# Performance work log

Hardware: AMD Instinct MI355X
Metric: run time of the kernel (lower is better)

The kernel has to match this reference:

```python
import jax, jax.numpy as jnp
import numpy as np

RX = (2, 9)
RY = (4, 9)
G, O = 64, 2          # column chunk size and overlap (hardcoded in original forward)
GK = RX[1]            # Gaussian (uniform box) kernel size, must be odd
M = N = 512


def _patches(x, kh, kw, pc, pr):
    # torch: F.pad(x,(pr,pr,pc,pc)).unfold(-2,kh,1).unfold(-2,kw,1).flatten(-2)
    xp = jnp.pad(x, ((0, 0), (0, 0), (pc, pc), (pr, pr)))
    p = jax.lax.conv_general_dilated_patches(xp, (kh, kw), (1, 1), 'VALID')  # (b, kh*kw, m, n) since c==1
    return jnp.moveaxis(p, 1, -1)[:, None]  # (b,1,m,n,kh*kw)


def _spatial_kernel(kh, kw):
    d = (jnp.arange(kh, dtype=jnp.float32) - kh // 2)[:, None] ** 2 \
        + (jnp.arange(kw, dtype=jnp.float32) - kw // 2)[None, :] ** 2
    return jnp.exp(-d.reshape(-1) / ((kh * kw) / 4.0) ** 2)


def _gen_weight(ych, kh, kw, pc, pr, sigma):
    p = _patches(ych, kh, kw, pc, pr)
    w = jnp.exp(-((p - ych[..., None]) ** 2) / (sigma / 2.0) ** 2)  # range (bilateral) term
    w = w * _spatial_kernel(kh, kw)                                  # spatial Gaussian term
    w = w * _patches(jnp.ones_like(ych), kh, kw, pc, pr)             # zero out padded taps
    return w / w.sum(-1, keepdims=True)


def _boxfilter(x, weight, kh, kw, pc, pr):
    return (_patches(x, kh, kw, pc, pr) * weight).sum(-1)


def _forward(X, y, r):
    sigma = r[0] * (y.max() - y.min())
    kh0, kw0, pc0, pr0 = 2 * RX[0] + 1, 2 * RY[0] + 1, RX[0], RY[0]  # detail kernel
    kh1, kw1, pc1, pr1 = 2 * RX[1] + 1, 2 * RY[1] + 1, RX[1], RY[1]  # base kernel
    gk = jnp.ones((1, 1, GK, GK), X.dtype) / float(GK * GK)
    pad = GK // 2
    conv = lambda z: jax.lax.conv_general_dilated(z, gk, (1, 1), [(pad, pad), (pad, pad)])

    # Angle = [0]: rotate(.,0,expand=True) and CenterCrop(m,n) are identities.
    XX, yy = X, y
    XXbase, yybase = conv(XX), conv(yy)
    XXdetail, yydetail = XX - XXbase, yy - yybase

    n = X.shape[-1]
    idx = np.arange(n)
    chunks = [idx[i:i + G] for i in range(0, n, G - O)]
    if len(chunks[-1]) <= 5:
        chunks[-2] = np.arange(chunks[-2][0], n)
        del chunks[-1]

    bdetail, Abase, bbase = [], [], []
    for index, ck in enumerate(chunks):
        s, e = int(ck[0]), int(ck[-1]) + 1
        Xb, Xd = XXbase[..., s:e], XXdetail[..., s:e]
        yb, yd = yybase[..., s:e], yydetail[..., s:e]
        wD = _gen_weight(Xd, kh0, kw0, pc0, pr0, sigma)
        wB = _gen_weight(Xb, kh1, kw1, pc1, pr1, sigma)
        lo = 0 if index == 0 else O // 2
        hi = None if index == len(chunks) - 1 else -(O // 2)
        bdetail.append(_boxfilter(yd - Xd, wD, kh0, kw0, pc0, pr0)[..., lo:hi])
        mean_y = _boxfilter(yb, wB, kh1, kw1, pc1, pr1)
        mean_x = _boxfilter(Xb, wB, kh1, kw1, pc1, pr1)
        var_x = _boxfilter(Xb * Xb, wB, kh1, kw1, pc1, pr1) - mean_x * mean_x
        cov_xy = _boxfilter(Xb * yb, wB, kh1, kw1, pc1, pr1) - mean_x * mean_y
        A = cov_xy / (var_x + 1e-6)
        b = mean_y - A * mean_x
        bbase.append(b[..., lo:hi])
        Abase.append(A[..., lo:hi])

    bdetail = jnp.concatenate(bdetail, -1)
    Abase = jnp.concatenate(Abase, -1)
    bbase = jnp.concatenate(bbase, -1)
    return Abase * XXbase + bbase + XXdetail + bdetail


def setup_inputs() -> dict:
    key = jax.random.key(0)
    k1, k2, k3 = jax.random.split(key, 3)
    X = jax.random.uniform(k1, (1, 1, M, N), dtype=jnp.float32)
    y = jax.random.uniform(k2, (1, 1, M, N), dtype=jnp.float32)
    r = jax.random.uniform(k3, (1,), dtype=jnp.float32)
    return {"X": X, "y": y, "r": r}


def reference(X, y, r):
    return _forward(X, y, r)
```

## Files before the change

### kernel.cpp

```cpp
#include <hip/hip_runtime.h>

#define W 512

__device__ __forceinline__ float fexp2(float x) {
#if __has_builtin(__builtin_amdgcn_exp2f)
    return __builtin_amdgcn_exp2f(x);
#else
    return __expf(x * 0.6931471805599453f);
#endif
}

__global__ __launch_bounds__(256) void k_minmax(const float* __restrict__ y,
                                                float2* __restrict__ partial) {
    __shared__ float smn[256], smx[256];
    int t = threadIdx.x;
    const float4* y4 = (const float4*)y;
    float4 v = y4[blockIdx.x * 256 + t];
    float mn = fminf(fminf(v.x, v.y), fminf(v.z, v.w));
    float mx = fmaxf(fmaxf(v.x, v.y), fmaxf(v.z, v.w));
    smn[t] = mn; smx[t] = mx;
    __syncthreads();
    for (int off = 128; off > 0; off >>= 1) {
        if (t < off) {
            smn[t] = fminf(smn[t], smn[t + off]);
            smx[t] = fmaxf(smx[t], smx[t + off]);
        }
        __syncthreads();
    }
    if (t == 0) partial[blockIdx.x] = make_float2(smn[0], smx[0]);
}

__global__ __launch_bounds__(256, 4) void k_fused(const float* __restrict__ X,
                                                  const float* __restrict__ y,
                                                  const float2* __restrict__ partial,
                                                  const float* __restrict__ r,
                                                  float* __restrict__ out) {
    __shared__ float sbx[19];
    __shared__ float sdy[5];
    __shared__ __align__(16) char ldsbuf[38624];
    float*  sX  = (float*)ldsbuf;
    float*  sY  = sX + 42 * 42;
    float*  csX = sY + 42 * 42;
    float*  csY = csX + 34 * 42;
    float2* bXY = (float2*)(csY + 34 * 42);
    float2* dXD = bXY + 34 * 34;
    float2* red = (float2*)sX;

    int tx = threadIdx.x, ty = threadIdx.y;
    int t = ty * 16 + tx;
    int c0 = blockIdx.x * 16, r0 = blockIdx.y * 16;

    if (t < 19)      { int d = t - 9;  sbx[t]      = __expf(-(float)(d * d) / 8145.0625f); }
    else if (t < 24) { int d = t - 21; sdy[t - 19] = __expf(-(float)(d * d) / 126.5625f); }

    red[t] = partial[t];
    __syncthreads();
    for (int off = 128; off > 0; off >>= 1) {
        if (t < off) {
            red[t].x = fminf(red[t].x, red[t + off].x);
            red[t].y = fmaxf(red[t].y, red[t + off].y);
        }
        __syncthreads();
    }
    float2 mm0 = red[0];
    __syncthreads();
    float sigma = r[0] * (mm0.y - mm0.x);
    float hh = 0.5f * sigma;
    float k2 = -1.4426950408889634f / (hh * hh);

    for (int i = t; i < 42 * 42; i += 256) {
        int rr = i / 42, cc2 = i - rr * 42;
        int gr = r0 - 13 + rr, gc = c0 - 13 + cc2;
        bool ok = ((unsigned)gr < 512u) & ((unsigned)gc < 512u);
        float xv = 0.f, yv = 0.f;
        if (ok) { xv = X[gr * W + gc]; yv = y[gr * W + gc]; }
        sX[i] = xv; sY[i] = yv;
    }
    __syncthreads();

    for (int i = t; i < 34 * 42; i += 256) {
        int rr = i / 42, cc2 = i - rr * 42;
        float ax = 0.f, ay = 0.f;
#pragma unroll
        for (int k = 0; k < 9; ++k) { ax += sX[(rr + k) * 42 + cc2]; ay += sY[(rr + k) * 42 + cc2]; }
        csX[i] = ax; csY[i] = ay;
    }
    __syncthreads();

    const float inv81 = 1.0f / 81.0f;
    for (int i = t; i < 34 * 34; i += 256) {
        int rr = i / 34, cc2 = i - rr * 34;
        float ax = 0.f, ay = 0.f;
#pragma unroll
        for (int k = 0; k < 9; ++k) { ax += csX[rr * 42 + cc2 + k]; ay += csY[rr * 42 + cc2 + k]; }
        bXY[i] = make_float2(ax * inv81, ay * inv81);
    }
    __syncthreads();

    for (int i = t; i < 20 * 24; i += 256) {
        int rr = i / 24, cc2 = i - rr * 24;
        float2 b2 = bXY[(rr + 7) * 34 + (cc2 + 5)];
        float xc = sX[(rr + 11) * 42 + (cc2 + 9)];
        float yc = sY[(rr + 11) * 42 + (cc2 + 9)];
        float xd = xc - b2.x;
        dXD[i] = make_float2(xd, (yc - b2.y) - xd);
    }
    __syncthreads();

    int c = c0 + tx;
    int h = r0 + ty;

    int chunk = (c == 0) ? 0 : (c - 1) / 62;
    if (chunk > 8) chunk = 8;
    int s = 62 * chunk;
    int e = (chunk == 8) ? 512 : (s + 64);

    const float ksb = -1.4426950408889634f / 8145.0625f;
    const float ksd = -1.4426950408889634f / 126.5625f;
    float cc[19];
#pragma unroll
    for (int j = 0; j < 19; ++j) {
        int nc = c - 9 + j, d = j - 9;
        cc[j] = ((nc >= s) & (nc < e)) ? ksb * (float)(d * d) : -1e30f;
    }
    float ccd[9];
#pragma unroll
    for (int j = 0; j < 9; ++j) {
        int nc = c - 4 + j, d = j - 4;
        ccd[j] = ((nc >= s) & (nc < e)) ? ksd * (float)(d * d) : -1e30f;
    }

    float Xc = bXY[(ty + 9) * 34 + tx + 9].x;
    float Xd = dXD[(ty + 2) * 24 + tx + 4].x;

    float sw = 0.f, swx = 0.f, swy = 0.f, swxx = 0.f, swxy = 0.f;
#pragma unroll 1
    for (int k = 0; k < 19; ++k) {
        int nh = h - 9 + k;
        if ((unsigned)nh >= 512u) continue;
        const float2* xr = bXY + (ty + k) * 34 + tx;
        float rs = 0.f, rsx = 0.f, rsy = 0.f, rsxx = 0.f, rsxy = 0.f;
#pragma unroll
        for (int j = 0; j < 19; ++j) {
            float2 v = xr[j];
            float u = v.x - Xc;
            float a = fmaf(u * k2, u, cc[j]);
            float w = fexp2(a);
            rs += w;
            rsx = fmaf(w, v.x, rsx);
            rsy = fmaf(w, v.y, rsy);
            float tt = w * v.x;
            rsxx = fmaf(tt, v.x, rsxx);
            rsxy = fmaf(tt, v.y, rsxy);
        }
        float ey = sbx[k];
        sw   = fmaf(ey, rs,   sw);
        swx  = fmaf(ey, rsx,  swx);
        swy  = fmaf(ey, rsy,  swy);
        swxx = fmaf(ey, rsxx, swxx);
        swxy = fmaf(ey, rsxy, swxy);
    }

    float swd = 0.f, sv = 0.f;
#pragma unroll 1
    for (int k = 0; k < 5; ++k) {
        int nh = h - 2 + k;
        if ((unsigned)nh >= 512u) continue;
        const float2* dr2 = dXD + (ty + k) * 24 + tx;
        float rs = 0.f, rv = 0.f;
#pragma unroll
        for (int j = 0; j < 9; ++j) {
            float2 v = dr2[j];
            float u = v.x - Xd;
            float a = fmaf(u * k2, u, ccd[j]);
            float w = fexp2(a);
            rs += w;
            rv = fmaf(w, v.y, rv);
        }
        swd = fmaf(sdy[k], rs, swd);
        sv  = fmaf(sdy[k], rv, sv);
    }

    float inv  = 1.0f / sw;
    float mx   = swx * inv, my = swy * inv;
    float varx = fmaf(-mx, mx, swxx * inv);
    float cov  = fmaf(-mx, my, swxy * inv);
    float A    = cov / (varx + 1e-6f);
    float b    = my - A * mx;
    float bd   = sv / swd;
    out[h * W + c] = fmaf(A, Xc, b) + Xd + bd;
}

extern "C" void kernel_launch(void* const* d_in, const int* in_sizes, int n_in,
                              void* d_out, int out_size, void* d_ws, size_t ws_size,
                              hipStream_t stream) {
    const float* X = (const float*)d_in[0];
    const float* y = (const float*)d_in[1];
    const float* r = (const float*)d_in[2];
    float* out = (float*)d_out;
    float2* partial = (float2*)d_ws;

    k_minmax<<<256, 256, 0, stream>>>(y, partial);
    k_fused<<<dim3(32, 32), dim3(16, 16), 0, stream>>>(X, y, partial, r, out);
}
```

Before: 95.50 us.

## Split fused kernel into box-filter precompute and bilateral kernels via global workspace

The single fused kernel is split in two. The first computes the 9x9 box-filtered base and detail planes once per pixel into global workspace and has one block reduce min/max into k2. The second loads halo tiles of those planes and runs the bilateral/guided accumulation. This removes the redundant halo box-filter work and the per-block min/max reduction, and cuts LDS use so more blocks can be resident. The cost is an extra launch and a global round-trip for the intermediates, with a fallback to the fused kernel when the workspace is too small.

```diff
diff --git a/kernel.cpp b/kernel.cpp
--- a/kernel.cpp
+++ b/kernel.cpp
@@ -28,6 +28,192 @@
         __syncthreads();
     }
     if (t == 0) partial[blockIdx.x] = make_float2(smn[0], smx[0]);
+}
+
+__global__ __launch_bounds__(256) void k_box(const float* __restrict__ X,
+                                             const float* __restrict__ y,
+                                             const float2* __restrict__ partial,
+                                             const float* __restrict__ r,
+                                             float2* __restrict__ bXY_g,
+                                             float2* __restrict__ dXD_g,
+                                             float* __restrict__ k2out) {
+    __shared__ __align__(16) float lds[1920];
+    float* sX  = lds;
+    float* sY  = sX + 576;
+    float* csX = sY + 576;
+    float* csY = csX + 384;
+
+    int tx = threadIdx.x, ty = threadIdx.y;
+    int t = ty * 16 + tx;
+    int c0 = blockIdx.x * 16, r0 = blockIdx.y * 16;
+
+    if (blockIdx.x == 0 && blockIdx.y == 0) {
+        float2* red = (float2*)lds;
+        red[t] = partial[t];
+        __syncthreads();
+        for (int off = 128; off > 0; off >>= 1) {
+            if (t < off) {
+                red[t].x = fminf(red[t].x, red[t + off].x);
+                red[t].y = fmaxf(red[t].y, red[t + off].y);
+            }
+            __syncthreads();
+        }
+        if (t == 0) {
+            float sigma = r[0] * (red[0].y - red[0].x);
+            float hh = 0.5f * sigma;
+            k2out[0] = -1.4426950408889634f / (hh * hh);
+        }
+        __syncthreads();
+    }
+
+    for (int i = t; i < 576; i += 256) {
+        int rr = i / 24, cc = i - rr * 24;
+        int gr = r0 - 4 + rr, gc = c0 - 4 + cc;
+        bool ok = ((unsigned)gr < 512u) & ((unsigned)gc < 512u);
+        float xv = 0.f, yv = 0.f;
+        if (ok) { xv = X[gr * W + gc]; yv = y[gr * W + gc]; }
+        sX[i] = xv; sY[i] = yv;
+    }
+    __syncthreads();
+
+    for (int i = t; i < 384; i += 256) {
+        int rr = i / 24, cc = i - rr * 24;
+        float ax = 0.f, ay = 0.f;
+#pragma unroll
+        for (int k = 0; k < 9; ++k) { ax += sX[(rr + k) * 24 + cc]; ay += sY[(rr + k) * 24 + cc]; }
+        csX[i] = ax; csY[i] = ay;
+    }
+    __syncthreads();
+
+    const float inv81 = 1.0f / 81.0f;
+    float ax = 0.f, ay = 0.f;
+#pragma unroll
+    for (int k = 0; k < 9; ++k) { ax += csX[ty * 24 + tx + k]; ay += csY[ty * 24 + tx + k]; }
+    float Xb = ax * inv81, yb = ay * inv81;
+    float xc = sX[(ty + 4) * 24 + tx + 4];
+    float yc = sY[(ty + 4) * 24 + tx + 4];
+    float xd = xc - Xb;
+    int p = (r0 + ty) * W + (c0 + tx);
+    bXY_g[p] = make_float2(Xb, yb);
+    dXD_g[p] = make_float2(xd, (yc - yb) - xd);
+}
+
+__global__ __launch_bounds__(256, 4) void k_bil(const float2* __restrict__ bXY_g,
+                                                const float2* __restrict__ dXD_g,
+                                                const float* __restrict__ k2buf,
+                                                float* __restrict__ out) {
+    __shared__ float sbx[19];
+    __shared__ float sdy[5];
+    __shared__ __align__(16) float2 bXYs[34 * 34];
+    __shared__ __align__(16) float2 dXDs[20 * 24];
+
+    int tx = threadIdx.x, ty = threadIdx.y;
+    int t = ty * 16 + tx;
+    int c0 = blockIdx.x * 16, r0 = blockIdx.y * 16;
+
+    if (t < 19)      { int d = t - 9;  sbx[t]      = __expf(-(float)(d * d) / 8145.0625f); }
+    else if (t < 24) { int d = t - 21; sdy[t - 19] = __expf(-(float)(d * d) / 126.5625f); }
+
+    float k2 = k2buf[0];
+
+    for (int i = t; i < 34 * 34; i += 256) {
+        int rr = i / 34, cc2 = i - rr * 34;
+        int gr = r0 - 9 + rr, gc = c0 - 9 + cc2;
+        float2 v = make_float2(0.f, 0.f);
+        if (((unsigned)gr < 512u) & ((unsigned)gc < 512u)) v = bXY_g[gr * W + gc];
+        bXYs[i] = v;
+    }
+    for (int i = t; i < 20 * 24; i += 256) {
+        int rr = i / 24, cc2 = i - rr * 24;
+        int gr = r0 - 2 + rr, gc = c0 - 4 + cc2;
+        float2 v = make_float2(0.f, 0.f);
+        if (((unsigned)gr < 512u) & ((unsigned)gc < 512u)) v = dXD_g[gr * W + gc];
+        dXDs[i] = v;
+    }
+    __syncthreads();
+
+    int c = c0 + tx;
+    int h = r0 + ty;
+
+    int chunk = (c == 0) ? 0 : (c - 1) / 62;
+    if (chunk > 8) chunk = 8;
+    int s = 62 * chunk;
+    int e = (chunk == 8) ? 512 : (s + 64);
+
+    const float ksb = -1.4426950408889634f / 8145.0625f;
+    const float ksd = -1.4426950408889634f / 126.5625f;
+    float cc[19];
+#pragma unroll
+    for (int j = 0; j < 19; ++j) {
+        int nc = c - 9 + j, d = j - 9;
+        cc[j] = ((nc >= s) & (nc < e)) ? ksb * (float)(d * d) : -1e30f;
+    }
+    float ccd[9];
+#pragma unroll
+    for (int j = 0; j < 9; ++j) {
+        int nc = c - 4 + j, d = j - 4;
+        ccd[j] = ((nc >= s) & (nc < e)) ? ksd * (float)(d * d) : -1e30f;
+    }
+
+    float Xc = bXYs[(ty + 9) * 34 + tx + 9].x;
+    float Xd = dXDs[(ty + 2) * 24 + tx + 4].x;
+
+    float sw = 0.f, swx = 0.f, swy = 0.f, swxx = 0.f, swxy = 0.f;
+#pragma unroll 1
+    for (int k = 0; k < 19; ++k) {
+        int nh = h - 9 + k;
+        if ((unsigned)nh >= 512u) continue;
+        const float2* xr = (const float2*)bXYs + (ty + k) * 34 + tx;
+        float rs = 0.f, rsx = 0.f, rsy = 0.f, rsxx = 0.f, rsxy = 0.f;
+#pragma unroll
+        for (int j = 0; j < 19; ++j) {
+            float2 v = xr[j];
+            float u = v.x - Xc;
+            float a = fmaf(u * k2, u, cc[j]);
+            float w = fexp2(a);
+            rs += w;
+            rsx = fmaf(w, v.x, rsx);
+            rsy = fmaf(w, v.y, rsy);
+            float tt = w * v.x;
+            rsxx = fmaf(tt, v.x, rsxx);
+            rsxy = fmaf(tt, v.y, rsxy);
+        }
+        float ey = sbx[k];
+        sw   = fmaf(ey, rs,   sw);
+        swx  = fmaf(ey, rsx,  swx);
+        swy  = fmaf(ey, rsy,  swy);
+        swxx = fmaf(ey, rsxx, swxx);
+        swxy = fmaf(ey, rsxy, swxy);
+    }
+
+    float swd = 0.f, sv = 0.f;
+#pragma unroll 1
+    for (int k = 0; k < 5; ++k) {
+        int nh = h - 2 + k;
+        if ((unsigned)nh >= 512u) continue;
+        const float2* dr2 = (const float2*)dXDs + (ty + k) * 24 + tx;
+        float rs = 0.f, rv = 0.f;
+#pragma unroll
+        for (int j = 0; j < 9; ++j) {
+            float2 v = dr2[j];
+            float u = v.x - Xd;
+            float a = fmaf(u * k2, u, ccd[j]);
+            float w = fexp2(a);
+            rs += w;
+            rv = fmaf(w, v.y, rv);
+        }
+        swd = fmaf(sdy[k], rs, swd);
+        sv  = fmaf(sdy[k], rv, sv);
+    }
+
+    float inv  = 1.0f / sw;
+    float mx   = swx * inv, my = swy * inv;
+    float varx = fmaf(-mx, mx, swxx * inv);
+    float cov  = fmaf(-mx, my, swxy * inv);
+    float A    = cov / (varx + 1e-6f);
+    float b    = my - A * mx;
+    float bd   = sv / swd;
+    out[h * W + c] = fmaf(A, Xc, b) + Xd + bd;
 }
 
 __global__ __launch_bounds__(256, 4) void k_fused(const float* __restrict__ X,
@@ -109,7 +295,6 @@
 
     int c = c0 + tx;
     int h = r0 + ty;
-
     int chunk = (c == 0) ? 0 : (c - 1) / 62;
     if (chunk > 8) chunk = 8;
     int s = 62 * chunk;
@@ -198,8 +383,18 @@
     const float* y = (const float*)d_in[1];
     const float* r = (const float*)d_in[2];
     float* out = (float*)d_out;
+
     float2* partial = (float2*)d_ws;
+    float*  k2buf   = (float*)((char*)d_ws + 2048);
+    float2* bXY_g   = (float2*)((char*)d_ws + 4096);
+    float2* dXD_g   = (float2*)((char*)d_ws + 4096 + 512 * 512 * 8);
+    size_t need = 4096 + (size_t)2 * 512 * 512 * 8;
 
     k_minmax<<<256, 256, 0, stream>>>(y, partial);
-    k_fused<<<dim3(32, 32), dim3(16, 16), 0, stream>>>(X, y, partial, r, out);
-}
+    if (ws_size >= need) {
+        k_box<<<dim3(32, 32), dim3(16, 16), 0, stream>>>(X, y, partial, r, bXY_g, dXD_g, k2buf);
+        k_bil<<<dim3(32, 32), dim3(16, 16), 0, stream>>>(bXY_g, dXD_g, k2buf, out);
+    } else {
+        k_fused<<<dim3(32, 32), dim3(16, 16), 0, stream>>>(X, y, partial, r, out);
+    }
+}
```

Measured after the change: 96.23 us. Within noise of the previous version (+0.8%).

## Vectorize bilateral inner loops with packed float2 math and split LDS planes

Applied to the files above, without the earlier changes.

Rewrites the 19x19 and 5x9 bilateral weight loops to process two taps at once using 2-wide vector types, so the compiler can emit packed FP32 instructions (v_pk_fma/v_pk_mul) and cut VALU instruction count. The interleaved float2 LDS arrays are split into separate X/Y planes padded to even widths, so pairs of adjacent taps can be loaded together. The min/max reduction of partials moves from a shared-memory tree with many barriers to a single-wave shuffle reduction. The exp2 calls stay scalar and there are extra padded taps and a final horizontal add. Register pressure may rise from the preloaded arrays.

```diff
diff --git a/kernel.cpp b/kernel.cpp
--- a/kernel.cpp
+++ b/kernel.cpp
@@ -1,6 +1,8 @@
 #include <hip/hip_runtime.h>
 
 #define W 512
+
+typedef float v2f __attribute__((ext_vector_type(2)));
 
 __device__ __forceinline__ float fexp2(float x) {
 #if __has_builtin(__builtin_amdgcn_exp2f)
@@ -9,6 +11,10 @@
     return __expf(x * 0.6931471805599453f);
 #endif
 }
+__device__ __forceinline__ v2f vfma(v2f a, v2f b, v2f c) {
+    return __builtin_elementwise_fma(a, b, c);
+}
+__device__ __forceinline__ v2f bc2(float x) { v2f r; r.x = x; r.y = x; return r; }
 
 __global__ __launch_bounds__(256) void k_minmax(const float* __restrict__ y,
                                                 float2* __restrict__ partial) {
@@ -37,14 +43,16 @@
                                                   float* __restrict__ out) {
     __shared__ float sbx[19];
     __shared__ float sdy[5];
-    __shared__ __align__(16) char ldsbuf[38624];
-    float*  sX  = (float*)ldsbuf;
-    float*  sY  = sX + 42 * 42;
-    float*  csX = sY + 42 * 42;
-    float*  csY = csX + 34 * 42;
-    float2* bXY = (float2*)(csY + 34 * 42);
-    float2* dXD = bXY + 34 * 34;
-    float2* red = (float2*)sX;
+    __shared__ float sk2;
+    __shared__ __align__(16) float arena[8832];
+    float* sX  = arena;
+    float* sY  = sX + 1764;
+    float* csX = sY + 1764;
+    float* csY = csX + 1428;
+    float* bX  = csY + 1428;
+    float* bY  = bX + 1224;
+    float* dX  = csX;
+    float* dD  = csX + 520;
 
     int tx = threadIdx.x, ty = threadIdx.y;
     int t = ty * 16 + tx;
@@ -53,57 +61,68 @@
     if (t < 19)      { int d = t - 9;  sbx[t]      = __expf(-(float)(d * d) / 8145.0625f); }
     else if (t < 24) { int d = t - 21; sdy[t - 19] = __expf(-(float)(d * d) / 126.5625f); }
 
-    red[t] = partial[t];
-    __syncthreads();
-    for (int off = 128; off > 0; off >>= 1) {
-        if (t < off) {
-            red[t].x = fminf(red[t].x, red[t + off].x);
-            red[t].y = fmaxf(red[t].y, red[t + off].y);
-        }
-        __syncthreads();
-    }
-    float2 mm0 = red[0];
-    __syncthreads();
-    float sigma = r[0] * (mm0.y - mm0.x);
-    float hh = 0.5f * sigma;
-    float k2 = -1.4426950408889634f / (hh * hh);
-
-    for (int i = t; i < 42 * 42; i += 256) {
-        int rr = i / 42, cc2 = i - rr * 42;
-        int gr = r0 - 13 + rr, gc = c0 - 13 + cc2;
+    if (t < 64) {
+        float2 p0 = partial[t], p1 = partial[t + 64], p2 = partial[t + 128], p3 = partial[t + 192];
+        float mn = fminf(fminf(p0.x, p1.x), fminf(p2.x, p3.x));
+        float mx = fmaxf(fmaxf(p0.y, p1.y), fmaxf(p2.y, p3.y));
+        for (int off = 32; off > 0; off >>= 1) {
+            mn = fminf(mn, __shfl_xor(mn, off));
+            mx = fmaxf(mx, __shfl_xor(mx, off));
+        }
+        if (t == 0) {
+            float sigma = r[0] * (mx - mn);
+            float hh = 0.5f * sigma;
+            sk2 = -1.4426950408889634f / (hh * hh);
+        }
+    }
+
+    for (int i = t; i < 1764; i += 256) {
+        int rr = i / 42, cc = i - rr * 42;
+        int gr = r0 - 13 + rr, gc = c0 - 13 + cc;
         bool ok = ((unsigned)gr < 512u) & ((unsigned)gc < 512u);
         float xv = 0.f, yv = 0.f;
         if (ok) { xv = X[gr * W + gc]; yv = y[gr * W + gc]; }
         sX[i] = xv; sY[i] = yv;
     }
     __syncthreads();
-
-    for (int i = t; i < 34 * 42; i += 256) {
-        int rr = i / 42, cc2 = i - rr * 42;
+    float k2 = sk2;
+    v2f k2v = bc2(k2);
+
+    for (int i = t; i < 1428; i += 256) {
+        int rr = i / 42, cc = i - rr * 42;
         float ax = 0.f, ay = 0.f;
 #pragma unroll
-        for (int k = 0; k < 9; ++k) { ax += sX[(rr + k) * 42 + cc2]; ay += sY[(rr + k) * 42 + cc2]; }
+        for (int k = 0; k < 9; ++k) { ax += sX[(rr + k) * 42 + cc]; ay += sY[(rr + k) * 42 + cc]; }
         csX[i] = ax; csY[i] = ay;
     }
     __syncthreads();
 
     const float inv81 = 1.0f / 81.0f;
-    for (int i = t; i < 34 * 34; i += 256) {
-        int rr = i / 34, cc2 = i - rr * 34;
-        float ax = 0.f, ay = 0.f;
-#pragma unroll
-        for (int k = 0; k < 9; ++k) { ax += csX[rr * 42 + cc2 + k]; ay += csY[rr * 42 + cc2 + k]; }
-        bXY[i] = make_float2(ax * inv81, ay * inv81);
-    }
-    __syncthreads();
-
-    for (int i = t; i < 20 * 24; i += 256) {
-        int rr = i / 24, cc2 = i - rr * 24;
-        float2 b2 = bXY[(rr + 7) * 34 + (cc2 + 5)];
-        float xc = sX[(rr + 11) * 42 + (cc2 + 9)];
-        float yc = sY[(rr + 11) * 42 + (cc2 + 9)];
-        float xd = xc - b2.x;
-        dXD[i] = make_float2(xd, (yc - b2.y) - xd);
+    for (int i = t; i < 1224; i += 256) {
+        int rr = i / 36, cc = i - rr * 36;
+        float bx = 0.f, by = 0.f;
+        if (cc < 34) {
+            float ax = 0.f, ay = 0.f;
+#pragma unroll
+            for (int k = 0; k < 9; ++k) { ax += csX[rr * 42 + cc + k]; ay += csY[rr * 42 + cc + k]; }
+            bx = ax * inv81; by = ay * inv81;
+        }
+        bX[i] = bx; bY[i] = by;
+    }
+    __syncthreads();
+
+    for (int i = t; i < 520; i += 256) {
+        int rr = i / 26, cc = i - rr * 26;
+        float xd = 0.f, dd = 0.f;
+        if (cc < 24) {
+            float Xb = bX[(rr + 7) * 36 + cc + 5];
+            float yb = bY[(rr + 7) * 36 + cc + 5];
+            float xc = sX[(rr + 11) * 42 + cc + 9];
+            float yc = sY[(rr + 11) * 42 + cc + 9];
+            xd = xc - Xb;
+            dd = (yc - yb) - xd;
+        }
+        dX[i] = xd; dD[i] = dd;
     }
     __syncthreads();
 
@@ -117,69 +136,97 @@
 
     const float ksb = -1.4426950408889634f / 8145.0625f;
     const float ksd = -1.4426950408889634f / 126.5625f;
-    float cc[19];
-#pragma unroll
-    for (int j = 0; j < 19; ++j) {
-        int nc = c - 9 + j, d = j - 9;
-        cc[j] = ((nc >= s) & (nc < e)) ? ksb * (float)(d * d) : -1e30f;
-    }
-    float ccd[9];
-#pragma unroll
-    for (int j = 0; j < 9; ++j) {
-        int nc = c - 4 + j, d = j - 4;
-        ccd[j] = ((nc >= s) & (nc < e)) ? ksd * (float)(d * d) : -1e30f;
-    }
-
-    float Xc = bXY[(ty + 9) * 34 + tx + 9].x;
-    float Xd = dXD[(ty + 2) * 24 + tx + 4].x;
-
-    float sw = 0.f, swx = 0.f, swy = 0.f, swxx = 0.f, swxy = 0.f;
+    v2f cp[10];
+#pragma unroll
+    for (int p = 0; p < 10; ++p) {
+        int j0 = 2 * p, j1 = 2 * p + 1;
+        int n0 = c - 9 + j0, d0 = j0 - 9;
+        int n1 = c - 9 + j1, d1 = j1 - 9;
+        cp[p].x = ((n0 >= s) & (n0 < e)) ? ksb * (float)(d0 * d0) : -1e30f;
+        cp[p].y = ((j1 < 19) & (n1 >= s) & (n1 < e)) ? ksb * (float)(d1 * d1) : -1e30f;
+    }
+    v2f cdp[5];
+#pragma unroll
+    for (int p = 0; p < 5; ++p) {
+        int j0 = 2 * p, j1 = 2 * p + 1;
+        int n0 = c - 4 + j0, d0 = j0 - 4;
+        int n1 = c - 4 + j1, d1 = j1 - 4;
+        cdp[p].x = ((n0 >= s) & (n0 < e)) ? ksd * (float)(d0 * d0) : -1e30f;
+        cdp[p].y = ((j1 < 9) & (n1 >= s) & (n1 < e)) ? ksd * (float)(d1 * d1) : -1e30f;
+    }
+
+    v2f Xc2 = bc2(bX[(ty + 9) * 36 + tx + 9]);
+    v2f Xd2 = bc2(dX[(ty + 2) * 26 + tx + 4]);
+
+    v2f s_w = bc2(0.f), s_wx = bc2(0.f), s_wy = bc2(0.f), s_wxx = bc2(0.f), s_wxy = bc2(0.f);
 #pragma unroll 1
     for (int k = 0; k < 19; ++k) {
         int nh = h - 9 + k;
         if ((unsigned)nh >= 512u) continue;
-        const float2* xr = bXY + (ty + k) * 34 + tx;
-        float rs = 0.f, rsx = 0.f, rsy = 0.f, rsxx = 0.f, rsxy = 0.f;
-#pragma unroll
-        for (int j = 0; j < 19; ++j) {
-            float2 v = xr[j];
-            float u = v.x - Xc;
-            float a = fmaf(u * k2, u, cc[j]);
-            float w = fexp2(a);
-            rs += w;
-            rsx = fmaf(w, v.x, rsx);
-            rsy = fmaf(w, v.y, rsy);
-            float tt = w * v.x;
-            rsxx = fmaf(tt, v.x, rsxx);
-            rsxy = fmaf(tt, v.y, rsxy);
-        }
-        float ey = sbx[k];
-        sw   = fmaf(ey, rs,   sw);
-        swx  = fmaf(ey, rsx,  swx);
-        swy  = fmaf(ey, rsy,  swy);
-        swxx = fmaf(ey, rsxx, swxx);
-        swxy = fmaf(ey, rsxy, swxy);
-    }
-
-    float swd = 0.f, sv = 0.f;
+        const float* xr = bX + (ty + k) * 36 + tx;
+        const float* yr = bY + (ty + k) * 36 + tx;
+        v2f xa[10], ya[10];
+#pragma unroll
+        for (int p = 0; p < 10; ++p) {
+            xa[p].x = xr[2 * p]; xa[p].y = xr[2 * p + 1];
+            ya[p].x = yr[2 * p]; ya[p].y = yr[2 * p + 1];
+        }
+        v2f rs = bc2(0.f), rsx = bc2(0.f), rsy = bc2(0.f), rsxx = bc2(0.f), rsxy = bc2(0.f);
+#pragma unroll
+        for (int p = 0; p < 10; ++p) {
+            v2f xv = xa[p], yv = ya[p];
+            v2f u = xv - Xc2;
+            v2f a = vfma(u * k2v, u, cp[p]);
+            v2f w; w.x = fexp2(a.x); w.y = fexp2(a.y);
+            v2f tt = w * xv;
+            rs = rs + w;
+            rsx = rsx + tt;
+            rsy  = vfma(w,  yv, rsy);
+            rsxx = vfma(tt, xv, rsxx);
+            rsxy = vfma(tt, yv, rsxy);
+        }
+        v2f eyv = bc2(sbx[k]);
+        s_w   = vfma(eyv, rs,   s_w);
+        s_wx  = vfma(eyv, rsx,  s_wx);
+        s_wy  = vfma(eyv, rsy,  s_wy);
+        s_wxx = vfma(eyv, rsxx, s_wxx);
+        s_wxy = vfma(eyv, rsxy, s_wxy);
+    }
+
+    v2f s_wd = bc2(0.f), s_v = bc2(0.f);
 #pragma unroll 1
     for (int k = 0; k < 5; ++k) {
         int nh = h - 2 + k;
         if ((unsigned)nh >= 512u) continue;
-        const float2* dr2 = dXD + (ty + k) * 24 + tx;
-        float rs = 0.f, rv = 0.f;
-#pragma unroll
-        for (int j = 0; j < 9; ++j) {
-            float2 v = dr2[j];
-            float u = v.x - Xd;
-            float a = fmaf(u * k2, u, ccd[j]);
-            float w = fexp2(a);
-            rs += w;
-            rv = fmaf(w, v.y, rv);
-        }
-        swd = fmaf(sdy[k], rs, swd);
-        sv  = fmaf(sdy[k], rv, sv);
-    }
+        const float* dr = dX + (ty + k) * 26 + tx;
+        const float* er = dD + (ty + k) * 26 + tx;
+        v2f xa[5], ea[5];
+#pragma unroll
+        for (int p = 0; p < 5; ++p) {
+            xa[p].x = dr[2 * p]; xa[p].y = dr[2 * p + 1];
+            ea[p].x = er[2 * p]; ea[p].y = er[2 * p + 1];
+        }
+        v2f rs = bc2(0.f), rv = bc2(0.f);
+#pragma unroll
+        for (int p = 0; p < 5; ++p) {
+            v2f u = xa[p] - Xd2;
+            v2f a = vfma(u * k2v, u, cdp[p]);
+            v2f w; w.x = fexp2(a.x); w.y = fexp2(a.y);
+            rs = rs + w;
+            rv = vfma(w, ea[p], rv);
+        }
+        v2f eyv = bc2(sdy[k]);
+        s_wd = vfma(eyv, rs, s_wd);
+        s_v  = vfma(eyv, rv, s_v);
+    }
+
+    float sw   = s_w.x + s_w.y;
+    float swx  = s_wx.x + s_wx.y;
+    float swy  = s_wy.x + s_wy.y;
+    float swxx = s_wxx.x + s_wxx.y;
+    float swxy = s_wxy.x + s_wxy.y;
+    float swd  = s_wd.x + s_wd.y;
+    float sv   = s_v.x + s_v.y;
 
     float inv  = 1.0f / sw;
     float mx   = swx * inv, my = swy * inv;
@@ -188,7 +235,7 @@
     float A    = cov / (varx + 1e-6f);
     float b    = my - A * mx;
     float bd   = sv / swd;
-    out[h * W + c] = fmaf(A, Xc, b) + Xd + bd;
+    out[h * W + c] = fmaf(A, Xc2.x, b) + Xd2.x + bd;
 }
 
 extern "C" void kernel_launch(void* const* d_in, const int* in_sizes, int n_in,
```

Result: no change. 95.41 us (-0.1%).
